# Performance work log

Hardware: AMD Instinct MI355X
Metric: run time of the kernel (lower is better)

## Reference

```python
import jax, jax.numpy as jnp
import numpy as np

M, B, D, Z, CH, K = 3, 8192, 2000, 256, 2, 40
F = Z // CH  # 128


def setup_inputs() -> dict:
    key = jax.random.key(0)
    ks = jax.random.split(key, 10)
    x = jax.random.normal(ks[0], (M, B, D), jnp.float32)
    # Stacked per-modality encoder weights (Linear+ReLU stack, dropout=0)
    enc_w0 = jax.random.normal(ks[1], (M, D, 1024), jnp.float32) * 0.02
    enc_b0 = jnp.zeros((M, 1024), jnp.float32)
    enc_w1 = jax.random.normal(ks[2], (M, 1024, 512), jnp.float32) * 0.02
    enc_b1 = jnp.zeros((M, 512), jnp.float32)
    enc_w2 = jax.random.normal(ks[3], (M, 512, Z), jnp.float32) * 0.02
    enc_b2 = jnp.zeros((M, Z), jnp.float32)
    # Attention params (torch.randn init in the original)
    aff = jax.random.normal(ks[4], (3, F, F), jnp.float32)      # C(3)=3 bilinear mats
    W = jax.random.normal(ks[5], (M, K, F), jnp.float32)
    Wh = jax.random.normal(ks[6], (M, M, K, 1), jnp.float32)
    return dict(x=x, enc_w0=enc_w0, enc_b0=enc_b0, enc_w1=enc_w1, enc_b1=enc_b1,
                enc_w2=enc_w2, enc_b2=enc_b2, aff=aff, W=W, Wh=Wh)


def reference(x, enc_w0, enc_b0, enc_w1, enc_b1, enc_w2, enc_b2, aff, W, Wh):
    # Encoders: Linear+ReLU x3, batched over modalities
    h = jax.nn.relu(jnp.einsum('mbd,mdh->mbh', x, enc_w0) + enc_b0[:, None, :])
    h = jax.nn.relu(jnp.einsum('mbd,mdh->mbh', h, enc_w1) + enc_b1[:, None, :])
    z = jax.nn.relu(jnp.einsum('mbd,mdh->mbh', h, enc_w2) + enc_b2[:, None, :])  # (M,B,Z)
    m, b = z.shape[0], z.shape[1]
    t = z.reshape(m, b, F, CH)  # (M,B,128,2), same layout as torch reshape

    # aff_weight index bookkeeping exactly as the original python loops:
    # per-row i, index starts at 0 and increments only after an i<j use.
    aff_idx = {}
    for i in range(m):
        idx = 0
        for j in range(i, m):
            aff_idx[(i, j)] = idx
            if i < j:
                idx += 1

    # affinity[i][j] = t_i^T @ aff @ t_j  -> (B,CH,CH)
    afm = {}
    for i in range(m):
        for j in range(i, m):
            afm[(i, j)] = jnp.einsum('bfc,fg,bgd->bcd', t[i], aff[aff_idx[(i, j)]], t[j])

    Wt = jnp.einsum('mkf,mbfc->mbkc', W, t)  # W[i] @ t_i, (M,B,K,CH)

    H = {}
    for i in range(m):
        for j in range(m):
            if i <= j:
                H[(i, j)] = jnp.tanh(Wt[j] + jnp.einsum('bkc,bcd->bkd', Wt[i], afm[(i, j)]))
            else:
                aff_ij = jnp.swapaxes(afm[(j, i)], 1, 2)
                H[(i, j)] = jnp.tanh(Wt[i] + jnp.einsum('bkc,bcd->bkd', Wt[j], aff_ij))

    outs = []
    for i in range(m):
        for j in range(m):
            if i != j:
                # A = softmax(W_h^T @ H) over the channel axis -> (B,CH)
                a = jax.nn.softmax(jnp.einsum('k,bkc->bc', Wh[i, j, :, 0], H[(i, j)]), axis=-1)
                outs.append((a[:, None, :] * t[i]).reshape(b, Z))
    concat_data = jnp.concatenate(outs, axis=1)  # (B, M*(M-1)*Z)
    return z, concat_data
```

## Files before the change

kernel.cpp:

```cpp
#include <hip/hip_runtime.h>

#define DEVI __device__ __forceinline__

typedef _Float16 f16;
typedef _Float16 f16x8 __attribute__((ext_vector_type(8)));
typedef float f32x4 __attribute__((ext_vector_type(4)));
typedef unsigned int u32;
typedef unsigned long long u64;

#define MM 3
#define BBATCH 8192
#define DDIM 2000
#define ZDIM 256
#define KATT 40
#define K0P 2048
#define N0 1024
#define N1 512
#define N2 256

typedef __attribute__((address_space(1))) u32 gu32;
typedef __attribute__((address_space(3))) u32 lu32;

DEVI void async16(const void* g, void* l) {
  __builtin_amdgcn_global_load_lds((const gu32*)g, (lu32*)l, 16, 0, 0);
}

__global__ void k_convx(const float* __restrict__ x, f16* __restrict__ xh) {
  const long long nch = (long long)MM * BBATCH * (K0P / 8);
  for (long long idx = (long long)blockIdx.x * blockDim.x + threadIdx.x; idx < nch;
       idx += (long long)gridDim.x * blockDim.x) {
    int c8 = (int)(idx & 255);
    long long row = idx >> 8;
    union { f16 h[8]; f16x8 v; } u;
    if (c8 < DDIM / 8) {
      const float* src = x + row * DDIM + c8 * 8;
      float4 a = *reinterpret_cast<const float4*>(src);
      float4 b = *reinterpret_cast<const float4*>(src + 4);
      u.h[0] = (f16)a.x; u.h[1] = (f16)a.y; u.h[2] = (f16)a.z; u.h[3] = (f16)a.w;
      u.h[4] = (f16)b.x; u.h[5] = (f16)b.y; u.h[6] = (f16)b.z; u.h[7] = (f16)b.w;
    } else {
      for (int j = 0; j < 8; ++j) u.h[j] = (f16)0.f;
    }
    *reinterpret_cast<f16x8*>(xh + row * K0P + c8 * 8) = u.v;
  }
}

__global__ void k_wt(const float* __restrict__ w, f16* __restrict__ wt, int K, int Kpad, int N) {
  __shared__ float tile[32][33];
  int m = blockIdx.z;
  int k0 = blockIdx.x * 32, n0 = blockIdx.y * 32;
  const float* wm = w + (long long)m * K * N;
  f16* wtm = wt + (long long)m * N * Kpad;
  for (int p = 0; p < 4; ++p) {
    int idx = threadIdx.x + p * 256;
    int kk = idx >> 5, nn = idx & 31;
    float v = 0.f;
    if (k0 + kk < K) v = wm[(long long)(k0 + kk) * N + n0 + nn];
    tile[kk][nn] = v;
  }
  __syncthreads();
  for (int p = 0; p < 4; ++p) {
    int idx = threadIdx.x + p * 256;
    int nn = idx >> 5, kk = idx & 31;
    wtm[(long long)(n0 + nn) * Kpad + k0 + kk] = (f16)tile[kk][nn];
  }
}

__global__ void k_convsmall(const float* __restrict__ aff, const float* __restrict__ W,
                            f16* __restrict__ affH, f16* __restrict__ WH) {
  int idx = blockIdx.x * 256 + threadIdx.x;
  if (idx < 2 * 128 * 128) affH[idx] = (f16)aff[idx];
  if (idx < 3 * 64 * 128) {
    int m = idx >> 13;
    int k = (idx >> 7) & 63;
    int f = idx & 127;
    WH[idx] = (k < KATT) ? (f16)W[(m * KATT + k) * 128 + f] : (f16)0.f;
  }
}

template <int OUTF16>
__global__ __launch_bounds__(256, 2) void k_gemm(const f16* __restrict__ A,
                                                 const f16* __restrict__ BT,
                                                 const float* __restrict__ bias,
                                                 f16* __restrict__ outh,
                                                 float* __restrict__ outf,
                                                 f16* __restrict__ tH, int K, int N) {
  __shared__ f16 As[128 * 64];
  __shared__ f16 Bs[128 * 64];
  const int m = blockIdx.z;
  const int gm0 = blockIdx.y * 128;
  const int gn0 = blockIdx.x * 128;
  const int tid = threadIdx.x;
  const int wave = tid >> 6, lane = tid & 63;
  const int wr = wave >> 1, wc = wave & 1;

  const f16* Am = A + (long long)m * BBATCH * K;
  const f16* Bm = BT + (long long)m * N * K;

  const int srow = wave * 32 + (lane >> 3);
  const int sslot = (lane & 7) ^ (lane >> 3);
  const f16* aSrc = Am + (long long)(gm0 + srow) * K + sslot * 8;
  const f16* bSrc = Bm + (long long)(gn0 + srow) * K + sslot * 8;
  char* AsB = (char*)As;
  char* BsB = (char*)Bs;

  f32x4 zero = {0.f, 0.f, 0.f, 0.f};
  f32x4 acc[4][4];
  for (int i = 0; i < 4; ++i)
    for (int j = 0; j < 4; ++j) acc[i][j] = zero;

  for (int kt = 0; kt < K; kt += 64) {
    if (kt) __syncthreads();
#pragma unroll
    for (int q = 0; q < 4; ++q) {
      async16(aSrc + (long long)q * 8 * K + kt, AsB + (wave * 32 + q * 8) * 128);
      async16(bSrc + (long long)q * 8 * K + kt, BsB + (wave * 32 + q * 8) * 128);
    }
    __syncthreads();
#pragma unroll
    for (int ks = 0; ks < 2; ++ks) {
      f16x8 af[4], bf[4];
#pragma unroll
      for (int i = 0; i < 4; ++i) {
        int row = wr * 64 + i * 16 + (lane & 15);
        int slot = (ks * 4 + (lane >> 4)) ^ (row & 7);
        af[i] = *reinterpret_cast<const f16x8*>(AsB + row * 128 + slot * 16);
      }
#pragma unroll
      for (int j = 0; j < 4; ++j) {
        int row = wc * 64 + j * 16 + (lane & 15);
        int slot = (ks * 4 + (lane >> 4)) ^ (row & 7);
        bf[j] = *reinterpret_cast<const f16x8*>(BsB + row * 128 + slot * 16);
      }
#pragma unroll
      for (int i = 0; i < 4; ++i)
#pragma unroll
        for (int j = 0; j < 4; ++j)
          acc[i][j] = __builtin_amdgcn_mfma_f32_16x16x32_f16(af[i], bf[j], acc[i][j], 0, 0, 0);
    }
  }

  const int rowl = (lane >> 4) * 4;
  const int coll = lane & 15;
  for (int j = 0; j < 4; ++j) {
    int col = gn0 + wc * 64 + j * 16 + coll;
    float bv = bias[m * N + col];
    for (int i = 0; i < 4; ++i) {
      int row0 = gm0 + wr * 64 + i * 16 + rowl;
      for (int r = 0; r < 4; ++r) {
        float v = acc[i][j][r] + bv;
        v = v > 0.f ? v : 0.f;
        if constexpr (OUTF16) {
          outh[((long long)m * BBATCH + row0 + r) * N + col] = (f16)v;
        } else {
          outf[((long long)m * BBATCH + row0 + r) * N + col] = v;
          tH[((long long)(m * BBATCH + row0 + r) * 2 + (col & 1)) * 128 + (col >> 1)] = (f16)v;
        }
      }
    }
  }
}

__global__ __launch_bounds__(256, 2) void k_sg(const f16* __restrict__ tH,
                                               const f16* __restrict__ affH,
                                               const f16* __restrict__ WH,
                                               f16* __restrict__ u, float* __restrict__ WtG) {
  __shared__ f16 As[128 * 128];
  __shared__ f16 Bs[128 * 128];
  const int zb = blockIdx.z;
  const int gm0 = blockIdx.y * 128;
  const bool isU = (zb < 3);
  const int p = isU ? zb : zb - 3;
  const int src = isU ? ((p == 0) ? 1 : 2) : p;
  const f16* Am = tH + (long long)src * 16384 * 128;
  const f16* Bm;
  int brows;
  if (isU) {
    int km = (p == 1) ? 1 : 0;
    Bm = affH + km * 128 * 128;
    brows = 128;
  } else {
    Bm = WH + p * 64 * 128;
    brows = 64;
  }

  const int tid = threadIdx.x;
  const int wave = tid >> 6, lane = tid & 63;
  const int wr = wave >> 1, wc = wave & 1;
  char* AsB = (char*)As;
  char* BsB = (char*)Bs;

#pragma unroll
  for (int q = 0; q < 8; ++q) {
    int sb = q * 4 + wave;
    int row = sb * 4 + (lane >> 4);
    int lsl = (lane & 15) ^ (row & 7);
    async16(Am + (long long)(gm0 + row) * 128 + lsl * 8, AsB + sb * 1024);
    if (sb * 4 < brows)
      async16(Bm + (long long)row * 128 + lsl * 8, BsB + sb * 1024);
  }
  if (brows == 64) {
    f16x8 z8 = {};
    for (int idx = tid; idx < 1024; idx += 256) {
      int row = 64 + (idx >> 4), sl = idx & 15;
      *reinterpret_cast<f16x8*>(BsB + row * 256 + sl * 16) = z8;
    }
  }
  __syncthreads();

  f32x4 zero = {0.f, 0.f, 0.f, 0.f};
  f32x4 acc[4][4];
  for (int i = 0; i < 4; ++i)
    for (int j = 0; j < 4; ++j) acc[i][j] = zero;

#pragma unroll
  for (int ks = 0; ks < 4; ++ks) {
    f16x8 af[4], bf[4];
#pragma unroll
    for (int i = 0; i < 4; ++i) {
      int row = wr * 64 + i * 16 + (lane & 15);
      int slot = (ks * 4 + (lane >> 4)) ^ (row & 7);
      af[i] = *reinterpret_cast<const f16x8*>(AsB + row * 256 + slot * 16);
    }
#pragma unroll
    for (int j = 0; j < 4; ++j) {
      int row = wc * 64 + j * 16 + (lane & 15);
      int slot = (ks * 4 + (lane >> 4)) ^ (row & 7);
      bf[j] = *reinterpret_cast<const f16x8*>(BsB + row * 256 + slot * 16);
    }
#pragma unroll
    for (int i = 0; i < 4; ++i)
#pragma unroll
      for (int j = 0; j < 4; ++j)
        acc[i][j] = __builtin_amdgcn_mfma_f32_16x16x32_f16(af[i], bf[j], acc[i][j], 0, 0, 0);
  }

  const int rowl = (lane >> 4) * 4;
  const int coll = lane & 15;
  if (isU) {
    for (int j = 0; j < 4; ++j) {
      int col = wc * 64 + j * 16 + coll;
      for (int i = 0; i < 4; ++i) {
        int row0 = gm0 + wr * 64 + i * 16 + rowl;
        for (int r = 0; r < 4; ++r)
          u[((long long)p * 16384 + row0 + r) * 128 + col] = (f16)acc[i][j][r];
      }
    }
  } else if (wc == 0) {
    for (int j = 0; j < 4; ++j) {
      int col = j * 16 + coll;
      for (int i = 0; i < 4; ++i) {
        int row0 = gm0 + wr * 64 + i * 16 + rowl;
        for (int r = 0; r < 4; ++r)
          WtG[((long long)p * 16384 + row0 + r) * 64 + col] = acc[i][j][r];
      }
    }
  }
}

DEVI float dot128(const f16* __restrict__ a, const f16* __restrict__ b) {
  float s = 0.f;
#pragma unroll
  for (int ch = 0; ch < 16; ++ch) {
    f16x8 av = *reinterpret_cast<const f16x8*>(a + ch * 8);
    f16x8 bv = *reinterpret_cast<const f16x8*>(b + ch * 8);
#pragma unroll
    for (int q = 0; q < 8; ++q) s += (float)av[q] * (float)bv[q];
  }
  return s;
}

DEVI float ftanh(float x) {
  x = fminf(fmaxf(x, -15.f), 15.f);
  float t = __expf(-2.f * x);
  return (1.f - t) / (1.f + t);
}

#define BB 32
__global__ void k_tail(const float* __restrict__ z, const f16* __restrict__ tH,
                       const f16* __restrict__ u, const float* __restrict__ WtG,
                       const float* __restrict__ Wh, float* __restrict__ out) {
  __shared__ float aa[BB][6][2];
  const int tid = threadIdx.x;
  const int bbase = blockIdx.x * BB;

  if (tid < BB * 6) {
    int bb = tid / 6, q = tid % 6;
    int b = bbase + bb;
    int i = q >> 1;
    int j = (q & 1) ? ((i == 2) ? 1 : 2) : ((i == 0) ? 1 : 0);
    int a = i < j ? i : j;
    int b2 = i < j ? j : i;
    int pidx = a + b2 - 1;
    bool trans = (i > j);

    float afm[2][2];
#pragma unroll
    for (int c = 0; c < 2; ++c)
#pragma unroll
      for (int d = 0; d < 2; ++d)
        afm[c][d] = dot128(tH + ((long long)(a * BBATCH + b) * 2 + c) * 128,
                           u + ((long long)pidx * 16384 + b * 2 + d) * 128);

    float m00, m01, m10, m11;
    if (!trans) { m00 = afm[0][0]; m01 = afm[0][1]; m10 = afm[1][0]; m11 = afm[1][1]; }
    else        { m00 = afm[0][0]; m01 = afm[1][0]; m10 = afm[0][1]; m11 = afm[1][1]; }

    const float* wb0 = WtG + ((long long)b2 * 16384 + b * 2 + 0) * 64;
    const float* wb1 = WtG + ((long long)b2 * 16384 + b * 2 + 1) * 64;
    const float* wa0 = WtG + ((long long)a * 16384 + b * 2 + 0) * 64;
    const float* wa1 = WtG + ((long long)a * 16384 + b * 2 + 1) * 64;
    const float* wh = Wh + (i * 3 + j) * KATT;
    float s0 = 0.f, s1 = 0.f;
    for (int k = 0; k < KATT; ++k) {
      float a0v = wa0[k], a1v = wa1[k];
      float h0 = ftanh(wb0[k] + a0v * m00 + a1v * m10);
      float h1 = ftanh(wb1[k] + a0v * m01 + a1v * m11);
      float w = wh[k];
      s0 += w * h0;
      s1 += w * h1;
    }
    float mx = fmaxf(s0, s1);
    float e0 = __expf(s0 - mx), e1 = __expf(s1 - mx);
    float inv = 1.f / (e0 + e1);
    aa[bb][q][0] = e0 * inv;
    aa[bb][q][1] = e1 * inv;
  }
  __syncthreads();

  for (int idx = tid; idx < BB * 6 * 256; idx += 256) {
    int zz = idx & 255;
    int r = idx >> 8;
    int q = r % 6;
    int bb = r / 6;
    int iM = q >> 1;
    float av = aa[bb][q][zz & 1];
    float tv = z[((long long)iM * BBATCH + bbase + bb) * ZDIM + zz];
    out[(long long)(bbase + bb) * 1536 + q * 256 + zz] = av * tv;
  }
}

extern "C" void kernel_launch(void* const* d_in, const int* in_sizes, int n_in, void* d_out,
                              int out_size, void* d_ws, size_t ws_size, hipStream_t stream) {
  const float* x = (const float*)d_in[0];
  const float* w0 = (const float*)d_in[1];
  const float* b0 = (const float*)d_in[2];
  const float* w1 = (const float*)d_in[3];
  const float* b1 = (const float*)d_in[4];
  const float* w2 = (const float*)d_in[5];
  const float* b2 = (const float*)d_in[6];
  const float* aff = (const float*)d_in[7];
  const float* W = (const float*)d_in[8];
  const float* Wh = (const float*)d_in[9];
  float* zout = (float*)d_out;
  float* cout = zout + (long long)MM * BBATCH * ZDIM;

  char* ws = (char*)d_ws;
  size_t off = 0;
  auto alloc = [&](size_t bytes) {
    char* p = ws + off;
    off += (bytes + 255) & ~(size_t)255;
    return p;
  };
  f16* xh = (f16*)alloc((size_t)MM * BBATCH * K0P * 2);
  f16* wT0 = (f16*)alloc((size_t)MM * N0 * K0P * 2);
  f16* wT1 = (f16*)alloc((size_t)MM * N1 * N0 * 2);
  f16* wT2 = (f16*)alloc((size_t)MM * N2 * N1 * 2);
  f16* h0 = (f16*)alloc((size_t)MM * BBATCH * N0 * 2);
  f16* h1 = (f16*)alloc((size_t)MM * BBATCH * N1 * 2);
  f16* affH = (f16*)alloc((size_t)2 * 128 * 128 * 2);
  f16* WH = (f16*)alloc((size_t)3 * 64 * 128 * 2);
  if (ws_size < off) return;

  f16* tH = (f16*)xh;
  f16* u = (f16*)((char*)xh + (size_t)3 * 16384 * 128 * 2);
  float* WtG = (float*)((char*)xh + (size_t)2 * 3 * 16384 * 128 * 2);

  k_convx<<<4096, 256, 0, stream>>>(x, xh);
  k_convsmall<<<128, 256, 0, stream>>>(aff, W, affH, WH);
  k_wt<<<dim3(K0P / 32, N0 / 32, 3), 256, 0, stream>>>(w0, wT0, DDIM, K0P, N0);
  k_wt<<<dim3(N0 / 32, N1 / 32, 3), 256, 0, stream>>>(w1, wT1, N0, N0, N1);
  k_wt<<<dim3(N1 / 32, N2 / 32, 3), 256, 0, stream>>>(w2, wT2, N1, N1, N2);
  k_gemm<1><<<dim3(N0 / 128, BBATCH / 128, 3), 256, 0, stream>>>(xh, wT0, b0, h0, nullptr, nullptr, K0P, N0);
  k_gemm<1><<<dim3(N1 / 128, BBATCH / 128, 3), 256, 0, stream>>>(h0, wT1, b1, h1, nullptr, nullptr, N0, N1);
  k_gemm<0><<<dim3(N2 / 128, BBATCH / 128, 3), 256, 0, stream>>>(h1, wT2, b2, nullptr, zout, tH, N1, N2);
  k_sg<<<dim3(1, 128, 6), 256, 0, stream>>>(tH, affH, WH, u, WtG);
  k_tail<<<256, 256, 0, stream>>>(zout, tH, u, WtG, Wh, cout);
}
```

Measured before the change: 314.3 us.

## Add 256x256-tile MFMA GEMM with 4-stage async LDS pipeline for encoder layers

```diff
diff --git a/kernel.cpp b/kernel.cpp
--- a/kernel.cpp
+++ b/kernel.cpp
@@ -20,10 +20,13 @@
 
 typedef __attribute__((address_space(1))) u32 gu32;
 typedef __attribute__((address_space(3))) u32 lu32;
+typedef __attribute__((address_space(3))) char lchar;
 
 DEVI void async16(const void* g, void* l) {
   __builtin_amdgcn_global_load_lds((const gu32*)g, (lu32*)l, 16, 0, 0);
 }
+
+DEVI u32 lds_u32(const char* p) { return (u32)(unsigned long long)(lchar*)p; }
 
 __global__ void k_convx(const float* __restrict__ x, f16* __restrict__ xh) {
   const long long nch = (long long)MM * BBATCH * (K0P / 8);
@@ -149,6 +152,161 @@
       int row0 = gm0 + wr * 64 + i * 16 + rowl;
       for (int r = 0; r < 4; ++r) {
         float v = acc[i][j][r] + bv;
+        v = v > 0.f ? v : 0.f;
+        if constexpr (OUTF16) {
+          outh[((long long)m * BBATCH + row0 + r) * N + col] = (f16)v;
+        } else {
+          outf[((long long)m * BBATCH + row0 + r) * N + col] = v;
+          tH[((long long)(m * BBATCH + row0 + r) * 2 + (col & 1)) * 128 + (col >> 1)] = (f16)v;
+        }
+      }
+    }
+  }
+}
+
+
+#define SYNCV(VMN)                                         \
+  asm volatile("s_waitcnt vmcnt(" #VMN ")" ::: "memory");  \
+  __builtin_amdgcn_s_barrier();
+
+#define LGKM12                                             \
+  asm volatile("s_waitcnt lgkmcnt(12)" ::: "memory");      \
+  __builtin_amdgcn_sched_barrier(0);
+
+#define LGKM0F                                             \
+  asm volatile("s_waitcnt lgkmcnt(0)" ::: "memory");       \
+  __builtin_amdgcn_sched_barrier(0);
+
+#define ENDBAR __builtin_amdgcn_s_barrier();
+
+#define RD1(D, A, OFF) \
+  asm volatile("ds_read_b128 %0, %1 offset:" #OFF : "=v"(D) : "v"(A));
+
+#define READ12(FA, FB, AA, AB)                                     \
+  RD1(FA[0], AA, 0)    RD1(FA[1], AA, 1024)                        \
+  RD1(FA[2], AA, 2048) RD1(FA[3], AA, 3072)                        \
+  RD1(FA[4], AA, 4096) RD1(FA[5], AA, 5120)                        \
+  RD1(FA[6], AA, 6144) RD1(FA[7], AA, 7168)                        \
+  RD1(FB[0], AB, 0)    RD1(FB[1], AB, 1024)                        \
+  RD1(FB[2], AB, 2048) RD1(FB[3], AB, 3072)
+
+#define MFMA32(FA, FB)                                             \
+  __builtin_amdgcn_s_setprio(1);                                   \
+  _Pragma("unroll") for (int mf = 0; mf < 8; ++mf)                 \
+  _Pragma("unroll") for (int nf = 0; nf < 4; ++nf)                 \
+    acc[mf][nf] = __builtin_amdgcn_mfma_f32_16x16x32_f16(          \
+        FA[mf], FB[nf], acc[mf][nf], 0, 0, 0);                     \
+  __builtin_amdgcn_s_setprio(0);
+
+#define PH_FULL(T, CA, CB, NA, NB)                                 \
+  {                                                                \
+    stage((T) + 3);                                                \
+    SYNCV(8)                                                       \
+    u32 aA = ldsb + (u32)((((T) + 1) & 3) * 32768) + baseA;        \
+    u32 aB = aA + (baseB - baseA);                                 \
+    READ12(NA, NB, aA, aB)                                         \
+    LGKM12                                                         \
+    MFMA32(CA, CB)                                                 \
+    ENDBAR                                                         \
+  }
+
+#define PH_NOST(T, CA, CB, NA, NB, VMS)                            \
+  {                                                                \
+    SYNCV(VMS)                                                     \
+    u32 aA = ldsb + (u32)((((T) + 1) & 3) * 32768) + baseA;        \
+    u32 aB = aA + (baseB - baseA);                                 \
+    READ12(NA, NB, aA, aB)                                         \
+    LGKM12                                                         \
+    MFMA32(CA, CB)                                                 \
+    ENDBAR                                                         \
+  }
+
+template <int OUTF16>
+__global__ __launch_bounds__(512, 1) void k_gemmt(const f16* __restrict__ A,
+                                                  const f16* __restrict__ BT,
+                                                  const float* __restrict__ bias,
+                                                  f16* __restrict__ outh,
+                                                  float* __restrict__ outf,
+                                                  f16* __restrict__ tH, int K, int N) {
+  extern __shared__ char lds[];
+  const int lin = blockIdx.y * gridDim.x + blockIdx.x;
+  const int cpx = (gridDim.x * gridDim.y) >> 3;
+  const int swz = (lin & 7) * cpx + (lin >> 3);
+  const int bx = swz % gridDim.x;
+  const int byy = swz / gridDim.x;
+  const int m = byy >> 5;
+  const int gm0 = (byy & 31) * 256;
+  const int gn0 = bx * 256;
+
+  const int tid = threadIdx.x;
+  const int wave = tid >> 6, lane = tid & 63;
+  const int wR = wave >> 2;
+  const int wC = wave & 3;
+  const int lrow = lane & 15;
+  const int l4 = lane >> 4;
+  const int slotr = l4 ^ ((lrow >> 1) & 3);
+
+  const f16* Am = A + (long long)m * BBATCH * K;
+  const f16* Bm = BT + (long long)m * N * K;
+  const int srow = tid >> 2;
+  const int sphys = tid & 3;
+  const int slog = sphys ^ ((srow >> 1) & 3);
+
+  auto stage = [&](int t) {
+    char* buf = lds + (t & 3) * 32768;
+    const long long kt = (long long)t << 5;
+    const f16* sa = Am + (long long)(gm0 + srow) * K + kt + slog * 8;
+    const f16* sb = Bm + (long long)(gn0 + srow) * K + kt + slog * 8;
+    char* da = buf + srow * 64 + sphys * 16;
+    async16(sa, da);
+    async16(sa + (long long)128 * K, da + 8192);
+    async16(sb, da + 16384);
+    async16(sb + (long long)128 * K, da + 16384 + 8192);
+  };
+
+  const u32 ldsb = lds_u32(lds);
+  const u32 baseA = (u32)((wR * 128 + lrow) * 64 + slotr * 16);
+  const u32 baseB = (u32)(16384 + (wC * 64 + lrow) * 64 + slotr * 16);
+
+  f16x8 frAa[8], frAb[4], frBa[8], frBb[4];
+  f32x4 acc[8][4];
+  f32x4 zero = {0.f, 0.f, 0.f, 0.f};
+#pragma unroll
+  for (int i = 0; i < 8; ++i)
+#pragma unroll
+    for (int j = 0; j < 4; ++j) acc[i][j] = zero;
+
+  const int NT = K >> 5;
+  stage(0); stage(1); stage(2);
+  SYNCV(8)
+  {
+    u32 aA = ldsb + baseA;
+    u32 aB = ldsb + baseB;
+    READ12(frAa, frAb, aA, aB)
+  }
+
+  for (int t = 0; t + 5 < NT; t += 2) {
+    PH_FULL(t, frAa, frAb, frBa, frBb)
+    PH_FULL(t + 1, frBa, frBb, frAa, frAb)
+  }
+  PH_FULL(NT - 4, frAa, frAb, frBa, frBb)
+  PH_NOST(NT - 3, frBa, frBb, frAa, frAb, 4)
+  PH_NOST(NT - 2, frAa, frAb, frBa, frBb, 0)
+  LGKM0F
+  MFMA32(frBa, frBb)
+
+  const int rowl = (lane >> 4) * 4;
+  const int coll = lane & 15;
+#pragma unroll
+  for (int nf = 0; nf < 4; ++nf) {
+    int col = gn0 + wC * 64 + nf * 16 + coll;
+    float bv = bias[m * N + col];
+#pragma unroll
+    for (int mf = 0; mf < 8; ++mf) {
+      int row0 = gm0 + wR * 128 + mf * 16 + rowl;
+#pragma unroll
+      for (int r = 0; r < 4; ++r) {
+        float v = acc[mf][nf][r] + bv;
         v = v > 0.f ? v : 0.f;
         if constexpr (OUTF16) {
           outh[((long long)m * BBATCH + row0 + r) * N + col] = (f16)v;
@@ -381,9 +539,21 @@
   k_wt<<<dim3(K0P / 32, N0 / 32, 3), 256, 0, stream>>>(w0, wT0, DDIM, K0P, N0);
   k_wt<<<dim3(N0 / 32, N1 / 32, 3), 256, 0, stream>>>(w1, wT1, N0, N0, N1);
   k_wt<<<dim3(N1 / 32, N2 / 32, 3), 256, 0, stream>>>(w2, wT2, N1, N1, N2);
-  k_gemm<1><<<dim3(N0 / 128, BBATCH / 128, 3), 256, 0, stream>>>(xh, wT0, b0, h0, nullptr, nullptr, K0P, N0);
-  k_gemm<1><<<dim3(N1 / 128, BBATCH / 128, 3), 256, 0, stream>>>(h0, wT1, b1, h1, nullptr, nullptr, N0, N1);
-  k_gemm<0><<<dim3(N2 / 128, BBATCH / 128, 3), 256, 0, stream>>>(h1, wT2, b2, nullptr, zout, tH, N1, N2);
+
+  const int LDST = 4 * 32768;
+  hipError_t e1 = hipFuncSetAttribute(reinterpret_cast<const void*>(&k_gemmt<1>),
+                                      hipFuncAttributeMaxDynamicSharedMemorySize, LDST);
+  hipError_t e2 = hipFuncSetAttribute(reinterpret_cast<const void*>(&k_gemmt<0>),
+                                      hipFuncAttributeMaxDynamicSharedMemorySize, LDST);
+  if (e1 == hipSuccess && e2 == hipSuccess) {
+    k_gemmt<1><<<dim3(N0 / 256, 96), 512, LDST, stream>>>(xh, wT0, b0, h0, nullptr, nullptr, K0P, N0);
+    k_gemmt<1><<<dim3(N1 / 256, 96), 512, LDST, stream>>>(h0, wT1, b1, h1, nullptr, nullptr, N0, N1);
+    k_gemmt<0><<<dim3(N2 / 256, 96), 512, LDST, stream>>>(h1, wT2, b2, nullptr, zout, tH, N1, N2);
+  } else {
+    k_gemm<1><<<dim3(N0 / 128, BBATCH / 128, 3), 256, 0, stream>>>(xh, wT0, b0, h0, nullptr, nullptr, K0P, N0);
+    k_gemm<1><<<dim3(N1 / 128, BBATCH / 128, 3), 256, 0, stream>>>(h0, wT1, b1, h1, nullptr, nullptr, N0, N1);
+    k_gemm<0><<<dim3(N2 / 128, BBATCH / 128, 3), 256, 0, stream>>>(h1, wT2, b2, nullptr, zout, tH, N1, N2);
+  }
   k_sg<<<dim3(1, 128, 6), 256, 0, stream>>>(tH, affH, WH, u, WtG);
   k_tail<<<256, 256, 0, stream>>>(zout, tH, u, WtG, Wh, cout);
 }
```

Measured after the change: 317.3 us. Within noise of the previous version (+0.9%).

## Fuse fp32-to-fp16 input conversion into first encoder GEMM A-tile load

Applied to the files above, without the earlier changes.

```diff
diff --git a/kernel.cpp b/kernel.cpp
--- a/kernel.cpp
+++ b/kernel.cpp
@@ -23,26 +23,6 @@
 
 DEVI void async16(const void* g, void* l) {
   __builtin_amdgcn_global_load_lds((const gu32*)g, (lu32*)l, 16, 0, 0);
-}
-
-__global__ void k_convx(const float* __restrict__ x, f16* __restrict__ xh) {
-  const long long nch = (long long)MM * BBATCH * (K0P / 8);
-  for (long long idx = (long long)blockIdx.x * blockDim.x + threadIdx.x; idx < nch;
-       idx += (long long)gridDim.x * blockDim.x) {
-    int c8 = (int)(idx & 255);
-    long long row = idx >> 8;
-    union { f16 h[8]; f16x8 v; } u;
-    if (c8 < DDIM / 8) {
-      const float* src = x + row * DDIM + c8 * 8;
-      float4 a = *reinterpret_cast<const float4*>(src);
-      float4 b = *reinterpret_cast<const float4*>(src + 4);
-      u.h[0] = (f16)a.x; u.h[1] = (f16)a.y; u.h[2] = (f16)a.z; u.h[3] = (f16)a.w;
-      u.h[4] = (f16)b.x; u.h[5] = (f16)b.y; u.h[6] = (f16)b.z; u.h[7] = (f16)b.w;
-    } else {
-      for (int j = 0; j < 8; ++j) u.h[j] = (f16)0.f;
-    }
-    *reinterpret_cast<f16x8*>(xh + row * K0P + c8 * 8) = u.v;
-  }
 }
 
 __global__ void k_wt(const float* __restrict__ w, f16* __restrict__ wt, int K, int Kpad, int N) {
@@ -75,6 +55,118 @@
     int k = (idx >> 7) & 63;
     int f = idx & 127;
     WH[idx] = (k < KATT) ? (f16)W[(m * KATT + k) * 128 + f] : (f16)0.f;
+  }
+}
+
+__global__ __launch_bounds__(256, 2) void k_gemmF(const float* __restrict__ A,
+                                                  const f16* __restrict__ BT,
+                                                  const float* __restrict__ bias,
+                                                  f16* __restrict__ outh) {
+  __shared__ f16 As[128 * 64];
+  __shared__ f16 Bs[128 * 64];
+  const int m = blockIdx.z;
+  const int gm0 = blockIdx.y * 128;
+  const int gn0 = blockIdx.x * 128;
+  const int tid = threadIdx.x;
+  const int wave = tid >> 6, lane = tid & 63;
+  const int wr = wave >> 1, wc = wave & 1;
+
+  const float* Am = A + (long long)m * BBATCH * DDIM;
+  const f16* Bm = BT + (long long)m * N0 * K0P;
+
+  const int srowB = wave * 32 + (lane >> 3);
+  const int sslotB = (lane & 7) ^ (lane >> 3);
+  const f16* bSrc = Bm + (long long)(gn0 + srowB) * K0P + sslotB * 8;
+  char* AsB = (char*)As;
+  char* BsB = (char*)Bs;
+
+  const int arow0 = wave * 32 + (lane >> 4);
+  const int akoff = (lane & 15) * 4;
+  const int asl = (lane & 15) >> 1;
+  const int abyte = (lane & 1) * 8;
+
+  float4 rA[8];
+  auto loadA = [&](int kt) {
+    const int k = kt + akoff;
+    const bool ok = k < DDIM;
+#pragma unroll
+    for (int q = 0; q < 8; ++q) {
+      if (ok)
+        rA[q] = *reinterpret_cast<const float4*>(Am + (long long)(gm0 + arow0 + q * 4) * DDIM + k);
+      else
+        rA[q] = make_float4(0.f, 0.f, 0.f, 0.f);
+    }
+  };
+  auto writeA = [&]() {
+#pragma unroll
+    for (int q = 0; q < 8; ++q) {
+      int row_t = arow0 + q * 4;
+      int phys = asl ^ (row_t & 7);
+      union { f16 h[4]; u64 d; } pk;
+      pk.h[0] = (f16)rA[q].x; pk.h[1] = (f16)rA[q].y;
+      pk.h[2] = (f16)rA[q].z; pk.h[3] = (f16)rA[q].w;
+      *reinterpret_cast<u64*>(AsB + row_t * 128 + phys * 16 + abyte) = pk.d;
+    }
+  };
+
+  f32x4 zero = {0.f, 0.f, 0.f, 0.f};
+  f32x4 acc[4][4];
+  for (int i = 0; i < 4; ++i)
+    for (int j = 0; j < 4; ++j) acc[i][j] = zero;
+
+  const int NT = K0P / 64;
+  loadA(0);
+  for (int t = 0; t < NT; ++t) {
+    if (t) __builtin_amdgcn_s_barrier();
+#pragma unroll
+    for (int q = 0; q < 4; ++q)
+      async16(bSrc + (long long)q * 8 * K0P + t * 64, BsB + (wave * 32 + q * 8) * 128);
+    __builtin_amdgcn_sched_barrier(0);
+    writeA();
+    if (t + 1 < NT) loadA((t + 1) * 64);
+    __builtin_amdgcn_sched_barrier(0);
+    if (t + 1 < NT) {
+      asm volatile("s_waitcnt vmcnt(8) lgkmcnt(0)" ::: "memory");
+    } else {
+      asm volatile("s_waitcnt vmcnt(0) lgkmcnt(0)" ::: "memory");
+    }
+    __builtin_amdgcn_s_barrier();
+#pragma unroll
+    for (int ks = 0; ks < 2; ++ks) {
+      f16x8 af[4], bf[4];
+#pragma unroll
+      for (int i = 0; i < 4; ++i) {
+        int row = wr * 64 + i * 16 + (lane & 15);
+        int slot = (ks * 4 + (lane >> 4)) ^ (row & 7);
+        af[i] = *reinterpret_cast<const f16x8*>(AsB + row * 128 + slot * 16);
+      }
+#pragma unroll
+      for (int j = 0; j < 4; ++j) {
+        int row = wc * 64 + j * 16 + (lane & 15);
+        int slot = (ks * 4 + (lane >> 4)) ^ (row & 7);
+        bf[j] = *reinterpret_cast<const f16x8*>(BsB + row * 128 + slot * 16);
+      }
+#pragma unroll
+      for (int i = 0; i < 4; ++i)
+#pragma unroll
+        for (int j = 0; j < 4; ++j)
+          acc[i][j] = __builtin_amdgcn_mfma_f32_16x16x32_f16(af[i], bf[j], acc[i][j], 0, 0, 0);
+    }
+  }
+
+  const int rowl = (lane >> 4) * 4;
+  const int coll = lane & 15;
+  for (int j = 0; j < 4; ++j) {
+    int col = gn0 + wc * 64 + j * 16 + coll;
+    float bv = bias[m * N0 + col];
+    for (int i = 0; i < 4; ++i) {
+      int row0 = gm0 + wr * 64 + i * 16 + rowl;
+      for (int r = 0; r < 4; ++r) {
+        float v = acc[i][j][r] + bv;
+        v = v > 0.f ? v : 0.f;
+        outh[((long long)m * BBATCH + row0 + r) * N0 + col] = (f16)v;
+      }
+    }
   }
 }
 
@@ -362,7 +454,7 @@
     off += (bytes + 255) & ~(size_t)255;
     return p;
   };
-  f16* xh = (f16*)alloc((size_t)MM * BBATCH * K0P * 2);
+  char* scratch = alloc((size_t)MM * BBATCH * K0P * 2);
   f16* wT0 = (f16*)alloc((size_t)MM * N0 * K0P * 2);
   f16* wT1 = (f16*)alloc((size_t)MM * N1 * N0 * 2);
   f16* wT2 = (f16*)alloc((size_t)MM * N2 * N1 * 2);
@@ -372,16 +464,16 @@
   f16* WH = (f16*)alloc((size_t)3 * 64 * 128 * 2);
   if (ws_size < off) return;
 
-  f16* tH = (f16*)xh;
-  f16* u = (f16*)((char*)xh + (size_t)3 * 16384 * 128 * 2);
-  float* WtG = (float*)((char*)xh + (size_t)2 * 3 * 16384 * 128 * 2);
-
-  k_convx<<<4096, 256, 0, stream>>>(x, xh);
+  f16* tH = (f16*)scratch;
+  f16* u = (f16*)(scratch + (size_t)3 * 16384 * 128 * 2);
+  float* WtG = (float*)(scratch + (size_t)2 * 3 * 16384 * 128 * 2);
+
   k_convsmall<<<128, 256, 0, stream>>>(aff, W, affH, WH);
   k_wt<<<dim3(K0P / 32, N0 / 32, 3), 256, 0, stream>>>(w0, wT0, DDIM, K0P, N0);
   k_wt<<<dim3(N0 / 32, N1 / 32, 3), 256, 0, stream>>>(w1, wT1, N0, N0, N1);
   k_wt<<<dim3(N1 / 32, N2 / 32, 3), 256, 0, stream>>>(w2, wT2, N1, N1, N2);
-  k_gemm<1><<<dim3(N0 / 128, BBATCH / 128, 3), 256, 0, stream>>>(xh, wT0, b0, h0, nullptr, nullptr, K0P, N0);
+
+  k_gemmF<<<dim3(N0 / 128, BBATCH / 128, 3), 256, 0, stream>>>(x, wT0, b0, h0);
   k_gemm<1><<<dim3(N1 / 128, BBATCH / 128, 3), 256, 0, stream>>>(h0, wT1, b1, h1, nullptr, nullptr, N0, N1);
   k_gemm<0><<<dim3(N2 / 128, BBATCH / 128, 3), 256, 0, stream>>>(h1, wT2, b2, nullptr, zout, tH, N1, N2);
   k_sg<<<dim3(1, 128, 6), 256, 0, stream>>>(tH, affH, WH, u, WtG);
```

Measured after the change: 402.3 us. +28.0%, slower.

## Add triple-buffered 256x128 GEMM kernel for first two encoder layers

Applied to the files above, without the earlier changes.

```diff
diff --git a/kernel.cpp b/kernel.cpp
--- a/kernel.cpp
+++ b/kernel.cpp
@@ -25,7 +25,17 @@
   __builtin_amdgcn_global_load_lds((const gu32*)g, (lu32*)l, 16, 0, 0);
 }
 
-__global__ void k_convx(const float* __restrict__ x, f16* __restrict__ xh) {
+__global__ void k_convx(const float* __restrict__ x, f16* __restrict__ xh,
+                        const float* __restrict__ aff, const float* __restrict__ W,
+                        f16* __restrict__ affH, f16* __restrict__ WH) {
+  int idx0 = blockIdx.x * 256 + threadIdx.x;
+  if (idx0 < 2 * 128 * 128) affH[idx0] = (f16)aff[idx0];
+  if (idx0 < 3 * 64 * 128) {
+    int m = idx0 >> 13;
+    int k = (idx0 >> 7) & 63;
+    int f = idx0 & 127;
+    WH[idx0] = (k < KATT) ? (f16)W[(m * KATT + k) * 128 + f] : (f16)0.f;
+  }
   const long long nch = (long long)MM * BBATCH * (K0P / 8);
   for (long long idx = (long long)blockIdx.x * blockDim.x + threadIdx.x; idx < nch;
        idx += (long long)gridDim.x * blockDim.x) {
@@ -63,18 +73,6 @@
     int idx = threadIdx.x + p * 256;
     int nn = idx >> 5, kk = idx & 31;
     wtm[(long long)(n0 + nn) * Kpad + k0 + kk] = (f16)tile[kk][nn];
-  }
-}
-
-__global__ void k_convsmall(const float* __restrict__ aff, const float* __restrict__ W,
-                            f16* __restrict__ affH, f16* __restrict__ WH) {
-  int idx = blockIdx.x * 256 + threadIdx.x;
-  if (idx < 2 * 128 * 128) affH[idx] = (f16)aff[idx];
-  if (idx < 3 * 64 * 128) {
-    int m = idx >> 13;
-    int k = (idx >> 7) & 63;
-    int f = idx & 127;
-    WH[idx] = (k < KATT) ? (f16)W[(m * KATT + k) * 128 + f] : (f16)0.f;
   }
 }
 
@@ -156,6 +154,114 @@
           outf[((long long)m * BBATCH + row0 + r) * N + col] = v;
           tH[((long long)(m * BBATCH + row0 + r) * 2 + (col & 1)) * 128 + (col >> 1)] = (f16)v;
         }
+      }
+    }
+  }
+}
+
+template <int OUTF16>
+__global__ __launch_bounds__(512, 1) void k_gemmt3(const f16* __restrict__ A,
+                                                   const f16* __restrict__ BT,
+                                                   const float* __restrict__ bias,
+                                                   f16* __restrict__ outh, int K, int N) {
+  extern __shared__ char lds[];
+  const int lin = blockIdx.y * gridDim.x + blockIdx.x;
+  const int cpx = (gridDim.x * gridDim.y) >> 3;
+  const int swz = (lin & 7) * cpx + (lin >> 3);
+  const int bx = swz % gridDim.x;
+  const int byy = swz / gridDim.x;
+  const int m = byy >> 5;
+  const int gm0 = (byy & 31) * 256;
+  const int gn0 = bx * 128;
+
+  const int tid = threadIdx.x;
+  const int wave = tid >> 6, lane = tid & 63;
+  const int wR = wave >> 1;
+  const int wC = wave & 1;
+  const int lrow = lane & 15;
+  const int l4 = lane >> 4;
+
+  const f16* Am = A + (long long)m * BBATCH * K;
+  const f16* Bm = BT + (long long)m * N * K;
+  const int srow = tid >> 3;
+  const int slog = (tid & 7) ^ (srow & 7);
+
+  auto stage = [&](int t) {
+    char* buf = lds + (t % 3) * 49152;
+    const long long kt = (long long)t << 6;
+    const f16* sa = Am + (long long)(gm0 + srow) * K + kt + slog * 8;
+    char* da = buf + srow * 128 + (tid & 7) * 16;
+#pragma unroll
+    for (int j = 0; j < 4; ++j) async16(sa + (long long)j * 64 * K, da + j * 8192);
+    const f16* sb = Bm + (long long)(gn0 + srow) * K + kt + slog * 8;
+    char* db = buf + 32768 + srow * 128 + (tid & 7) * 16;
+    async16(sb, db);
+    async16(sb + (long long)64 * K, db + 8192);
+  };
+
+  f16x8 af[2][4], bf[2][4];
+  f32x4 acc[4][4];
+  f32x4 zero = {0.f, 0.f, 0.f, 0.f};
+#pragma unroll
+  for (int i = 0; i < 4; ++i)
+#pragma unroll
+    for (int j = 0; j < 4; ++j) acc[i][j] = zero;
+
+  const int NT = K >> 6;
+  stage(0);
+  stage(1);
+
+  for (int u = 0; u < NT; ++u) {
+    if (u < NT - 1) {
+      asm volatile("s_waitcnt vmcnt(6)" ::: "memory");
+    } else {
+      asm volatile("s_waitcnt vmcnt(0)" ::: "memory");
+    }
+    __builtin_amdgcn_s_barrier();
+    __builtin_amdgcn_sched_barrier(0);
+    const char* bufA = lds + (u % 3) * 49152;
+    const char* bufB = bufA + 32768;
+    if (u + 2 < NT) stage(u + 2);
+#pragma unroll
+    for (int ks = 0; ks < 2; ++ks) {
+#pragma unroll
+      for (int mf = 0; mf < 4; ++mf) {
+        int row = wR * 64 + mf * 16 + lrow;
+        int slot = ((ks * 4 + l4) ^ (row & 7)) * 16;
+        af[ks][mf] = *reinterpret_cast<const f16x8*>(bufA + row * 128 + slot);
+      }
+#pragma unroll
+      for (int nf = 0; nf < 4; ++nf) {
+        int row = wC * 64 + nf * 16 + lrow;
+        int slot = ((ks * 4 + l4) ^ (row & 7)) * 16;
+        bf[ks][nf] = *reinterpret_cast<const f16x8*>(bufB + row * 128 + slot);
+      }
+    }
+    __builtin_amdgcn_s_setprio(1);
+#pragma unroll
+    for (int ks = 0; ks < 2; ++ks)
+#pragma unroll
+      for (int mf = 0; mf < 4; ++mf)
+#pragma unroll
+        for (int nf = 0; nf < 4; ++nf)
+          acc[mf][nf] = __builtin_amdgcn_mfma_f32_16x16x32_f16(af[ks][mf], bf[ks][nf], acc[mf][nf], 0, 0, 0);
+    __builtin_amdgcn_s_setprio(0);
+  }
+
+  const int rowl = (lane >> 4) * 4;
+  const int coll = lane & 15;
+#pragma unroll
+  for (int nf = 0; nf < 4; ++nf) {
+    int col = gn0 + wC * 64 + nf * 16 + coll;
+    float bv = bias[m * N + col];
+#pragma unroll
+    for (int mf = 0; mf < 4; ++mf) {
+      int row0 = gm0 + wR * 64 + mf * 16 + rowl;
+#pragma unroll
+      for (int r = 0; r < 4; ++r) {
+        float v = acc[mf][nf][r] + bv;
+        v = v > 0.f ? v : 0.f;
+        outh[((long long)m * BBATCH + row0 + r) * N + col] = (f16)v;
       }
     }
   }
@@ -376,13 +482,21 @@
   f16* u = (f16*)((char*)xh + (size_t)3 * 16384 * 128 * 2);
   float* WtG = (float*)((char*)xh + (size_t)2 * 3 * 16384 * 128 * 2);
 
-  k_convx<<<4096, 256, 0, stream>>>(x, xh);
-  k_convsmall<<<128, 256, 0, stream>>>(aff, W, affH, WH);
+  k_convx<<<4096, 256, 0, stream>>>(x, xh, aff, W, affH, WH);
   k_wt<<<dim3(K0P / 32, N0 / 32, 3), 256, 0, stream>>>(w0, wT0, DDIM, K0P, N0);
   k_wt<<<dim3(N0 / 32, N1 / 32, 3), 256, 0, stream>>>(w1, wT1, N0, N0, N1);
   k_wt<<<dim3(N1 / 32, N2 / 32, 3), 256, 0, stream>>>(w2, wT2, N1, N1, N2);
-  k_gemm<1><<<dim3(N0 / 128, BBATCH / 128, 3), 256, 0, stream>>>(xh, wT0, b0, h0, nullptr, nullptr, K0P, N0);
-  k_gemm<1><<<dim3(N1 / 128, BBATCH / 128, 3), 256, 0, stream>>>(h0, wT1, b1, h1, nullptr, nullptr, N0, N1);
+
+  const int LDST3 = 3 * 49152;
+  hipError_t e1 = hipFuncSetAttribute(reinterpret_cast<const void*>(&k_gemmt3<1>),
+                                      hipFuncAttributeMaxDynamicSharedMemorySize, LDST3);
+  if (e1 == hipSuccess) {
+    k_gemmt3<1><<<dim3(N0 / 128, 96), 512, LDST3, stream>>>(xh, wT0, b0, h0, K0P, N0);
+    k_gemmt3<1><<<dim3(N1 / 128, 96), 512, LDST3, stream>>>(h0, wT1, b1, h1, N0, N1);
+  } else {
+    k_gemm<1><<<dim3(N0 / 128, BBATCH / 128, 3), 256, 0, stream>>>(xh, wT0, b0, h0, nullptr, nullptr, K0P, N0);
+    k_gemm<1><<<dim3(N1 / 128, BBATCH / 128, 3), 256, 0, stream>>>(h0, wT1, b1, h1, nullptr, nullptr, N0, N1);
+  }
   k_gemm<0><<<dim3(N2 / 128, BBATCH / 128, 3), 256, 0, stream>>>(h1, wT2, b2, nullptr, zout, tH, N1, N2);
   k_sg<<<dim3(1, 128, 6), 256, 0, stream>>>(tH, affH, WH, u, WtG);
   k_tail<<<256, 256, 0, stream>>>(zout, tH, u, WtG, Wh, cout);
```

Measured after the change: 304.3 us. 1.03x faster.
